# Kernel tuning notes

Measured on AMD Instinct MI355X. Metric: run time of the kernel, lower is better.

Reference implementation:

```python
import jax, jax.numpy as jnp
import numpy as np

D_MODEL = 1024
N_HEADS = 16
HEAD_DIM = D_MODEL // N_HEADS  # 64


def _rotate_half(x):
    x1, x2 = jnp.split(x, 2, axis=-1)
    return jnp.concatenate((-x2, x1), axis=-1)


def setup_inputs() -> dict:
    key = jax.random.key(0)
    ks = jax.random.split(key, 9)
    B, S = 2, 2048
    sc = 1.0 / np.sqrt(D_MODEL)
    return {
        "x": jax.random.normal(ks[0], (B, S, D_MODEL), dtype=jnp.float32),
        "Wq": jax.random.normal(ks[1], (D_MODEL, D_MODEL), dtype=jnp.float32) * sc,
        "bq": jax.random.normal(ks[2], (D_MODEL,), dtype=jnp.float32) * 0.02,
        "Wk": jax.random.normal(ks[3], (D_MODEL, D_MODEL), dtype=jnp.float32) * sc,
        "bk": jax.random.normal(ks[4], (D_MODEL,), dtype=jnp.float32) * 0.02,
        "Wv": jax.random.normal(ks[5], (D_MODEL, D_MODEL), dtype=jnp.float32) * sc,
        "bv": jax.random.normal(ks[6], (D_MODEL,), dtype=jnp.float32) * 0.02,
        "Wo": jax.random.normal(ks[7], (D_MODEL, D_MODEL), dtype=jnp.float32) * sc,
        "bo": jax.random.normal(ks[8], (D_MODEL,), dtype=jnp.float32) * 0.02,
    }


def reference(x, Wq, bq, Wk, bk, Wv, bv, Wo, bo):
    B, S, _ = x.shape
    H, D = N_HEADS, HEAD_DIM
    # QKV projections -> [B, H, S, D]
    q = (x @ Wq + bq).reshape(B, S, H, D).transpose(0, 2, 1, 3)
    k = (x @ Wk + bk).reshape(B, S, H, D).transpose(0, 2, 1, 3)
    v = (x @ Wv + bv).reshape(B, S, H, D).transpose(0, 2, 1, 3)
    # Rotary embedding on head_dim
    inv_freq = 1.0 / (10000.0 ** (jnp.arange(0, D, 2, dtype=jnp.float32) / D))
    t = jnp.arange(S, dtype=jnp.float32)
    freqs = jnp.outer(t, inv_freq)                      # [S, D/2]
    emb = jnp.concatenate((freqs, freqs), axis=-1)      # [S, D]
    # Faithful to torch: cos/sin end up rank-5 [1,1,1,S,D], promoting q/k to [1,B,H,S,D]
    cos = jnp.cos(emb)[None, None, None]
    sin = jnp.sin(emb)[None, None, None]
    qe = q * cos + _rotate_half(q) * sin                # [1,B,H,S,D]
    ke = k * cos + _rotate_half(k) * sin                # [1,B,H,S,D]
    scores = jnp.matmul(qe, jnp.swapaxes(ke, -1, -2)) / np.sqrt(D).astype(np.float32)  # [1,B,H,S,S]
    attn = jax.nn.softmax(scores, axis=-1)
    out = jnp.matmul(attn, v)                           # [1,B,H,S,D] (v broadcast)
    # Faithful replication of torch transpose(1,2).contiguous().view(B,S,d_model)
    out = out.transpose(0, 2, 1, 3, 4).reshape(B, S, H * D)
    return out @ Wo + bo
```

## Files before the change

### kernel.cpp

```cpp
#include <hip/hip_runtime.h>
#include <hip/hip_bf16.h>
#include <stdint.h>

typedef __bf16 bf16;
typedef __bf16 bf16x8 __attribute__((ext_vector_type(8)));
typedef __bf16 bf16x4 __attribute__((ext_vector_type(4)));
typedef float  f32x4  __attribute__((ext_vector_type(4)));
typedef int    i32x4  __attribute__((ext_vector_type(4)));

#define MFMA16(a, b, c) __builtin_amdgcn_mfma_f32_16x16x32_bf16((a), (b), (c), 0, 0, 0)

#define GLOAD16(gp, lp) __builtin_amdgcn_global_load_lds(                     \
    (__attribute__((address_space(1))) void*)(gp),                            \
    (__attribute__((address_space(3))) void*)(lp), 16, 0, 0)


__global__ __launch_bounds__(256) void k_prep(
    const float* __restrict__ x,
    const float* __restrict__ Wq, const float* __restrict__ Wk,
    const float* __restrict__ Wv, const float* __restrict__ Wo,
    bf16* __restrict__ xb, bf16* __restrict__ wqkvt, bf16* __restrict__ wot,
    float* __restrict__ ct, float* __restrict__ st) {
    __shared__ float t[32][33];
    const int bid = blockIdx.x, tid = threadIdx.x;
    if (bid < 4096) {
        const int i = bid * 256 + tid;
        float4 v = ((const float4*)x)[i];
        bf16x4 o;
        o[0] = (bf16)v.x; o[1] = (bf16)v.y; o[2] = (bf16)v.z; o[3] = (bf16)v.w;
        ((bf16x4*)xb)[i] = o;
    } else if (bid < 4352) {
        const int i = (bid - 4096) * 256 + tid;
        const int s = i >> 5, j = i & 31;
        const float inv = expf(-(float)j * (9.210340371976184f / 32.0f));
        const float a = (float)s * inv;
        ct[i] = cosf(a);
        st[i] = sinf(a);
    } else {
        const int wb = bid - 4352;
        const int z = wb >> 10, tb = wb & 1023;
        const float* src = (z == 0) ? Wq : (z == 1) ? Wk : (z == 2) ? Wv : Wo;
        bf16* dst = (z < 3) ? wqkvt + (size_t)z * 1024 * 1024 : wot;
        const int bx = (tb & 31) * 32, by = (tb >> 5) * 32;
        const int tx = tid & 31, ty = tid >> 5;
#pragma unroll
        for (int i = 0; i < 32; i += 8)
            t[ty + i][tx] = src[(size_t)(by + ty + i) * 1024 + bx + tx];
        __syncthreads();
#pragma unroll
        for (int i = 0; i < 32; i += 8)
            dst[(size_t)(bx + ty + i) * 1024 + by + tx] = (bf16)t[tx][ty + i];
    }
}

__device__ __forceinline__ void gemm_loop(const bf16* __restrict__ A,
                                          const bf16* __restrict__ Bt,
                                          int m0, int n0,
                                          bf16* As, bf16* Bs,
                                          f32x4 (&acc)[4][4]) {
    const int tid  = threadIdx.x;
    const int w    = tid >> 6, lane = tid & 63;
    const int wr   = (w >> 1) * 64, wc = (w & 1) * 64;
    const int l15  = lane & 15, l4 = lane >> 4;
    const int srow = w * 16 + (lane >> 2);
    const int skol = 8 * ((lane & 3) ^ ((lane >> 3) & 3));
    const int rdb  = l15 * 32 + 8 * (l4 ^ ((l15 >> 1) & 3));
    const bf16* Ap = A  + (size_t)(m0 + srow) * 1024 + skol;
    const bf16* Bp = Bt + (size_t)(n0 + srow) * 1024 + skol;

#define GSTAGE(B, kt) do {                                                   \
        GLOAD16(Ap + (kt),         As + (B) * 4096 + w * 512);               \
        GLOAD16(Ap + 65536 + (kt), As + (B) * 4096 + 2048 + w * 512);        \
        GLOAD16(Bp + (kt),         Bs + (B) * 4096 + w * 512);               \
        GLOAD16(Bp + 65536 + (kt), Bs + (B) * 4096 + 2048 + w * 512);        \
    } while (0)

#define GCOMP(B) do {                                                        \
        bf16x8 af[4], bfv[4];                                                \
        _Pragma("unroll")                                                    \
        for (int m = 0; m < 4; ++m)                                          \
            af[m] = *(const bf16x8*)(As + (B) * 4096 + (wr + 16 * m) * 32 + rdb); \
        _Pragma("unroll")                                                    \
        for (int n = 0; n < 4; ++n)                                          \
            bfv[n] = *(const bf16x8*)(Bs + (B) * 4096 + (wc + 16 * n) * 32 + rdb); \
        __builtin_amdgcn_s_setprio(1);                                       \
        _Pragma("unroll")                                                    \
        for (int m = 0; m < 4; ++m)                                          \
            _Pragma("unroll")                                                \
            for (int n = 0; n < 4; ++n)                                      \
                acc[m][n] = MFMA16(af[m], bfv[n], acc[m][n]);                \
        __builtin_amdgcn_s_setprio(0);                                       \
    } while (0)

    GSTAGE(0, 0);
    GSTAGE(1, 32);
    for (int i = 0; i < 30; i += 3) {
        asm volatile("s_waitcnt vmcnt(8)" ::: "memory");
        __builtin_amdgcn_s_barrier();
        GSTAGE(2, (i + 2) * 32);
        GCOMP(0);
        asm volatile("s_waitcnt vmcnt(8)" ::: "memory");
        __builtin_amdgcn_s_barrier();
        GSTAGE(0, (i + 3) * 32);
        GCOMP(1);
        asm volatile("s_waitcnt vmcnt(8)" ::: "memory");
        __builtin_amdgcn_s_barrier();
        GSTAGE(1, (i + 4) * 32);
        GCOMP(2);
    }
    asm volatile("s_waitcnt vmcnt(8)" ::: "memory");
    __builtin_amdgcn_s_barrier();
    GCOMP(0);
    asm volatile("s_waitcnt vmcnt(0)" ::: "memory");
    __builtin_amdgcn_s_barrier();
    GCOMP(1);
#undef GCOMP
#undef GSTAGE
}

__global__ __launch_bounds__(256) void k_gemm_qkv(
    const bf16* __restrict__ X, const bf16* __restrict__ Wt,
    const float* __restrict__ bq, const float* __restrict__ bk,
    const float* __restrict__ bv,
    const float* __restrict__ ct, const float* __restrict__ st,
    bf16* __restrict__ qbuf, bf16* __restrict__ kbuf, bf16* __restrict__ vtb) {
    __shared__ __align__(16) bf16 As[3 * 4096];
    __shared__ __align__(16) bf16 Bs[3 * 4096];
    f32x4 acc[4][4] = {};
    const int nwg = gridDim.x * gridDim.y;
    const int wg  = blockIdx.y * gridDim.x + blockIdx.x;
    const int sw  = (wg & 7) * (nwg >> 3) + (wg >> 3);
    const int m0 = (sw / gridDim.x) * 128, n0 = (sw % gridDim.x) * 128;
    gemm_loop(X, Wt, m0, n0, As, Bs, acc);

    const int tid = threadIdx.x;
    const int w = tid >> 6, lane = tid & 63;
    const int wr = (w >> 1) * 64, wc = (w & 1) * 64;
    const int l15 = lane & 15, l4 = lane >> 4;

    const int featbase = n0 + wc;
    const int kind = featbase >> 10;
    const int col0 = featbase & 1023;
    const int h = col0 >> 6;
    const float* bias = (kind == 0) ? bq : (kind == 1) ? bk : bv;
    const float oscale = (kind == 0) ? 0.18033688011112042f : 1.0f;

#pragma unroll
    for (int m = 0; m < 4; ++m) {
#pragma unroll
        for (int j = 0; j < 4; ++j) {
            const int tok = m0 + wr + 16 * m + 4 * l4 + j;
            const int b = tok >> 11, s = tok & 2047;
            float vals[4];
#pragma unroll
            for (int n = 0; n < 4; ++n)
                vals[n] = acc[m][n][j] + bias[col0 + 16 * n + l15];
            if (kind < 2) {
                bf16* dst = (kind == 0) ? qbuf : kbuf;
                const size_t base = ((size_t)((b * 16 + h) * 2048 + s)) * 64;
#pragma unroll
                for (int n = 0; n < 4; ++n) {
                    const int dd = 16 * n + l15;
                    const int jr = dd & 31;
                    const float c = ct[s * 32 + jr], sn = st[s * 32 + jr];
                    const float other = vals[n ^ 2];
                    const float rot = (dd < 32) ? -other : other;
                    dst[base + dd] = (bf16)((vals[n] * c + rot * sn) * oscale);
                }
            } else {
                const int sp = (s & ~63) | ((s & 0x1C) << 1) | ((s & 0x20) >> 3) | (s & 3);
#pragma unroll
                for (int n = 0; n < 4; ++n) {
                    const int dd = 16 * n + l15;
                    vtb[((size_t)((b * 16 + h) * 64 + dd)) * 2048 + sp] = (bf16)vals[n];
                }
            }
        }
    }
}

__global__ __launch_bounds__(512) void k_attn(const bf16* __restrict__ qbuf,
                                              const bf16* __restrict__ kbuf,
                                              const bf16* __restrict__ vtb,
                                              bf16* __restrict__ ob) {
    __shared__ __align__(16) bf16 smem[2 * 2 * 2 * 4096];

    const int tid = threadIdx.x, w = tid >> 6, lane = tid & 63;
    const int team = w >> 2, wt = w & 3;
    const int l15 = lane & 15, l4 = lane >> 4;

    const int sid = blockIdx.x;
    const int bh  = (sid & 7) * 4 + ((sid >> 3) >> 4);
    const int qb0 = ((sid >> 3) & 15) * 128;
    const int b = bh >> 4, h = bh & 15;

    const bf16* qp = qbuf + ((size_t)bh * 2048 + qb0 + wt * 32 + l15) * 64 + 8 * l4;
    i32x4 qr00 = *(const i32x4*)qp;
    i32x4 qr01 = *(const i32x4*)(qp + 32);
    i32x4 qr10 = *(const i32x4*)(qp + 16 * 64);
    i32x4 qr11 = *(const i32x4*)(qp + 16 * 64 + 32);
    asm volatile("" :: "v"(qr00), "v"(qr01), "v"(qr10), "v"(qr11));
    asm volatile("s_waitcnt vmcnt(0)" ::: "memory");
    bf16x8 aq[2][2];
    aq[0][0] = __builtin_bit_cast(bf16x8, qr00);
    aq[0][1] = __builtin_bit_cast(bf16x8, qr01);
    aq[1][0] = __builtin_bit_cast(bf16x8, qr10);
    aq[1][1] = __builtin_bit_cast(bf16x8, qr11);

    bf16x8 ones;
#pragma unroll
    for (int i = 0; i < 8; ++i) ones[i] = (bf16)1.0f;

    f32x4 ao[2][4] = {};
    f32x4 lacc[2] = {};
    const f32x4 zf = {0.f, 0.f, 0.f, 0.f};

    const int r8   = lane >> 3;
    const int skol = 8 * ((lane & 7) ^ r8);
    const int rdb  = l15 * 64 + 32 * ((l15 >> 2) & 1) + 8 * (l4 ^ (l15 & 3));
    const bf16* kp = kbuf + (size_t)bh * 131072 + (size_t)team * 65536
                   + (size_t)(wt * 8 + r8) * 64 + skol;
    const bf16* vp = vtb  + (size_t)bh * 131072 + (size_t)(wt * 8 + r8) * 2048
                   + team * 1024 + skol;
    bf16* sK = smem + team * 16384;
    bf16* sV = smem + team * 16384 + 8192;
    const bf16* pK0 = sK + rdb;
    const bf16* pK1 = sK + (rdb ^ 32);
    const bf16* pV0 = sV + rdb;
    const bf16* pV1 = sV + (rdb ^ 32);

#define STAGE(B, t) do {                                                  \
        GLOAD16(kp + (size_t)(t) * 4096,        sK + (B) * 4096 + wt * 512);        \
        GLOAD16(kp + (size_t)(t) * 4096 + 2048, sK + (B) * 4096 + 2048 + wt * 512); \
        GLOAD16(vp + (t) * 64,                  sV + (B) * 4096 + wt * 512);        \
        GLOAD16(vp + 65536 + (t) * 64,          sV + (B) * 4096 + 2048 + wt * 512); \
    } while (0)

#define TILE(t, B) do {                                                       \
        asm volatile("s_waitcnt vmcnt(0)" ::: "memory");                      \
        __builtin_amdgcn_s_barrier();                                         \
        if ((t) < 15) STAGE((B) ^ 1, (t) + 1);                                \
        bf16x8 kfr[2][4], vfr[2][4];                                          \
        _Pragma("unroll")                                                     \
        for (int n = 0; n < 4; ++n) {                                         \
            kfr[0][n] = *(const bf16x8*)(pK0 + (B) * 4096 + n * 1024);        \
            kfr[1][n] = *(const bf16x8*)(pK1 + (B) * 4096 + n * 1024);        \
            vfr[0][n] = *(const bf16x8*)(pV0 + (B) * 4096 + n * 1024);        \
            vfr[1][n] = *(const bf16x8*)(pV1 + (B) * 4096 + n * 1024);        \
        }                                                                     \
        f32x4 sc[2][4];                                                       \
        __builtin_amdgcn_s_setprio(1);                                        \
        _Pragma("unroll")                                                     \
        for (int n = 0; n < 4; ++n) {                                         \
            sc[0][n] = MFMA16(kfr[0][n], aq[0][0], zf);                       \
            sc[1][n] = MFMA16(kfr[0][n], aq[1][0], zf);                       \
        }                                                                     \
        _Pragma("unroll")                                                     \
        for (int n = 0; n < 4; ++n) {                                         \
            sc[0][n] = MFMA16(kfr[1][n], aq[0][1], sc[0][n]);                 \
            sc[1][n] = MFMA16(kfr[1][n], aq[1][1], sc[1][n]);                 \
        }                                                                     \
        __builtin_amdgcn_s_setprio(0);                                        \
                  \
        bf16x8 ap[2][2];                                                      \
        _Pragma("unroll")                                                     \
        for (int f = 0; f < 2; ++f) {                                         \
            float e0[4], e1[4], e2[4], e3[4];                                 \
            _Pragma("unroll")                                                 \
            for (int r = 0; r < 4; ++r) {                                     \
                asm("v_exp_f32 %0, %1" : "=v"(e0[r]) : "v"(sc[f][0][r]));     \
                asm("v_exp_f32 %0, %1" : "=v"(e1[r]) : "v"(sc[f][1][r]));     \
                asm("v_exp_f32 %0, %1" : "=v"(e2[r]) : "v"(sc[f][2][r]));     \
                asm("v_exp_f32 %0, %1" : "=v"(e3[r]) : "v"(sc[f][3][r]));     \
            }                                                                 \
            unsigned q0, q1, q2, q3, q4, q5, q6, q7;                          \
            asm("v_cvt_pk_bf16_f32 %0, %1, %2" : "=v"(q0) : "v"(e0[0]), "v"(e0[1])); \
            asm("v_cvt_pk_bf16_f32 %0, %1, %2" : "=v"(q1) : "v"(e0[2]), "v"(e0[3])); \
            asm("v_cvt_pk_bf16_f32 %0, %1, %2" : "=v"(q2) : "v"(e2[0]), "v"(e2[1])); \
            asm("v_cvt_pk_bf16_f32 %0, %1, %2" : "=v"(q3) : "v"(e2[2]), "v"(e2[3])); \
            asm("v_cvt_pk_bf16_f32 %0, %1, %2" : "=v"(q4) : "v"(e1[0]), "v"(e1[1])); \
            asm("v_cvt_pk_bf16_f32 %0, %1, %2" : "=v"(q5) : "v"(e1[2]), "v"(e1[3])); \
            asm("v_cvt_pk_bf16_f32 %0, %1, %2" : "=v"(q6) : "v"(e3[0]), "v"(e3[1])); \
            asm("v_cvt_pk_bf16_f32 %0, %1, %2" : "=v"(q7) : "v"(e3[2]), "v"(e3[3])); \
            i32x4 w0 = {(int)q0, (int)q1, (int)q2, (int)q3};                  \
            i32x4 w1 = {(int)q4, (int)q5, (int)q6, (int)q7};                  \
            ap[f][0] = __builtin_bit_cast(bf16x8, w0);                        \
            ap[f][1] = __builtin_bit_cast(bf16x8, w1);                        \
        }                                                                     \
        __builtin_amdgcn_s_setprio(1);                                        \
        lacc[0] = MFMA16(ap[0][0], ones, lacc[0]);                            \
        lacc[0] = MFMA16(ap[0][1], ones, lacc[0]);                            \
        lacc[1] = MFMA16(ap[1][0], ones, lacc[1]);                            \
        lacc[1] = MFMA16(ap[1][1], ones, lacc[1]);                            \
        _Pragma("unroll")                                                     \
        for (int kk = 0; kk < 2; ++kk)                                        \
            _Pragma("unroll")                                                 \
            for (int n = 0; n < 4; ++n) {                                     \
                ao[0][n] = MFMA16(ap[0][kk], vfr[kk][n], ao[0][n]);           \
                ao[1][n] = MFMA16(ap[1][kk], vfr[kk][n], ao[1][n]);           \
            }                                                                 \
        __builtin_amdgcn_s_setprio(0);                                        \
    } while (0)

    STAGE(0, 0);
    for (int t = 0; t < 16; t += 2) {
        TILE(t, 0);
        TILE(t + 1, 1);
    }
#undef TILE
#undef STAGE

    float* mO = (float*)(smem + 16384);
    float* mL = (float*)smem;
    __syncthreads();
    if (team == 1) {
#pragma unroll
        for (int f = 0; f < 2; ++f) {
#pragma unroll
            for (int j = 0; j < 4; ++j) {
                const int row = wt * 32 + f * 16 + 4 * l4 + j;
#pragma unroll
                for (int n = 0; n < 4; ++n)
                    mO[row * 64 + 16 * n + l15] = ao[f][n][j];
                if (l15 == 0) mL[row] = lacc[f][j];
            }
        }
    }
    __syncthreads();
    if (team == 0) {
#pragma unroll
        for (int f = 0; f < 2; ++f) {
#pragma unroll
            for (int j = 0; j < 4; ++j) {
                const int row = wt * 32 + f * 16 + 4 * l4 + j;
                const float inv = 1.0f / (lacc[f][j] + mL[row]);
                const int s = qb0 + row;
                const size_t base = ((size_t)(h * 256 + b * 128 + (s >> 4))) * 1024
                                  + (s & 15) * 64;
#pragma unroll
                for (int n = 0; n < 4; ++n)
                    ob[base + 16 * n + l15] =
                        (bf16)((ao[f][n][j] + mO[row * 64 + 16 * n + l15]) * inv);
            }
        }
    }
}

__global__ __launch_bounds__(256) void k_gemm_out(const bf16* __restrict__ O,
                                                  const bf16* __restrict__ Wt,
                                                  const float* __restrict__ bo,
                                                  float* __restrict__ out) {
    __shared__ __align__(16) bf16 As[3 * 4096];
    __shared__ __align__(16) bf16 Bs[3 * 4096];
    f32x4 acc[4][4] = {};
    const int nwg = gridDim.x * gridDim.y;
    const int wg  = blockIdx.y * gridDim.x + blockIdx.x;
    const int sw  = (wg & 7) * (nwg >> 3) + (wg >> 3);
    const int m0 = (sw / gridDim.x) * 128, n0 = (sw % gridDim.x) * 128;
    gemm_loop(O, Wt, m0, n0, As, Bs, acc);

    const int tid = threadIdx.x;
    const int w = tid >> 6, lane = tid & 63;
    const int wr = (w >> 1) * 64, wc = (w & 1) * 64;
    const int l15 = lane & 15, l4 = lane >> 4;
#pragma unroll
    for (int m = 0; m < 4; ++m) {
#pragma unroll
        for (int j = 0; j < 4; ++j) {
            const int tok = m0 + wr + 16 * m + 4 * l4 + j;
#pragma unroll
            for (int n = 0; n < 4; ++n) {
                const int feat = n0 + wc + 16 * n + l15;
                out[(size_t)tok * 1024 + feat] = acc[m][n][j] + bo[feat];
            }
        }
    }
}

extern "C" void kernel_launch(void* const* d_in, const int* in_sizes, int n_in,
                              void* d_out, int out_size, void* d_ws, size_t ws_size,
                              hipStream_t stream) {
    (void)in_sizes; (void)n_in; (void)out_size; (void)ws_size;
    const float* x  = (const float*)d_in[0];
    const float* Wq = (const float*)d_in[1];
    const float* bq = (const float*)d_in[2];
    const float* Wk = (const float*)d_in[3];
    const float* bk = (const float*)d_in[4];
    const float* Wv = (const float*)d_in[5];
    const float* bv = (const float*)d_in[6];
    const float* Wo = (const float*)d_in[7];
    const float* bo = (const float*)d_in[8];
    float* out = (float*)d_out;

    char* p = (char*)d_ws;
    bf16* xb    = (bf16*)p;  p += (size_t)4096 * 1024 * 2;
    bf16* wqkvt = (bf16*)p;  p += (size_t)3072 * 1024 * 2;
    bf16* wot   = (bf16*)p;  p += (size_t)1024 * 1024 * 2;
    bf16* qbuf  = (bf16*)p;  p += (size_t)32 * 2048 * 64 * 2;
    bf16* kbuf  = (bf16*)p;  p += (size_t)32 * 2048 * 64 * 2;
    bf16* vtb   = (bf16*)p;  p += (size_t)32 * 64 * 2048 * 2;
    float* ct   = (float*)p; p += (size_t)2048 * 32 * 4;
    float* st   = (float*)p; p += (size_t)2048 * 32 * 4;
    bf16* obuf  = xb;

    k_prep<<<dim3(8448), dim3(256), 0, stream>>>(x, Wq, Wk, Wv, Wo,
                                                 xb, wqkvt, wot, ct, st);
    k_gemm_qkv<<<dim3(24, 32), dim3(256), 0, stream>>>(xb, wqkvt, bq, bk, bv,
                                                       ct, st, qbuf, kbuf, vtb);
    k_attn<<<dim3(512), dim3(512), 0, stream>>>(qbuf, kbuf, vtb, obuf);
    k_gemm_out<<<dim3(8, 32), dim3(256), 0, stream>>>(obuf, wot, bo, out);
}
```

Measured before the change: 118.8 us.

## Widen QKV GEMM tile to 128x256 with per-wave 128x64 subtiles

Replaces the shared gemm_loop in the QKV projection with a dedicated 128x256 tile loop. Each wave now computes all 128 rows for its own 64-column slice, so the grid is halved to 12x32 blocks. Every wave keeps 8x4 accumulators and reads all A fragments from shared memory. The aim is to raise arithmetic intensity and reuse of A per loaded tile. The cost is more registers and LDS per block, fewer blocks, and lower occupancy, which could hurt the load balance across the 256 CUs.

```diff
diff --git a/kernel.cpp b/kernel.cpp
--- a/kernel.cpp
+++ b/kernel.cpp
@@ -125,20 +125,75 @@
     const float* __restrict__ ct, const float* __restrict__ st,
     bf16* __restrict__ qbuf, bf16* __restrict__ kbuf, bf16* __restrict__ vtb) {
     __shared__ __align__(16) bf16 As[3 * 4096];
-    __shared__ __align__(16) bf16 Bs[3 * 4096];
-    f32x4 acc[4][4] = {};
+    __shared__ __align__(16) bf16 Bs[3 * 8192];
+    f32x4 acc[8][4] = {};
+
     const int nwg = gridDim.x * gridDim.y;
     const int wg  = blockIdx.y * gridDim.x + blockIdx.x;
     const int sw  = (wg & 7) * (nwg >> 3) + (wg >> 3);
-    const int m0 = (sw / gridDim.x) * 128, n0 = (sw % gridDim.x) * 128;
-    gemm_loop(X, Wt, m0, n0, As, Bs, acc);
-
-    const int tid = threadIdx.x;
-    const int w = tid >> 6, lane = tid & 63;
-    const int wr = (w >> 1) * 64, wc = (w & 1) * 64;
-    const int l15 = lane & 15, l4 = lane >> 4;
-
-    const int featbase = n0 + wc;
+    const int n0 = (sw % gridDim.x) * 256, m0 = (sw / gridDim.x) * 128;
+
+    const int tid  = threadIdx.x;
+    const int w    = tid >> 6, lane = tid & 63;
+    const int l15  = lane & 15, l4 = lane >> 4;
+    const int srow = w * 16 + (lane >> 2);
+    const int skol = 8 * ((lane & 3) ^ ((lane >> 3) & 3));
+    const int rdb  = l15 * 32 + 8 * (l4 ^ ((l15 >> 1) & 3));
+    const bf16* Ap = X  + (size_t)(m0 + srow) * 1024 + skol;
+    const bf16* Bp = Wt + (size_t)(n0 + srow) * 1024 + skol;
+
+#define WSTAGE(B, kt) do {                                                   \
+        GLOAD16(Ap + (kt),          As + (B) * 4096 + w * 512);              \
+        GLOAD16(Ap + 65536 + (kt),  As + (B) * 4096 + 2048 + w * 512);       \
+        GLOAD16(Bp + (kt),          Bs + (B) * 8192 + w * 512);              \
+        GLOAD16(Bp + 65536 + (kt),  Bs + (B) * 8192 + 2048 + w * 512);       \
+        GLOAD16(Bp + 131072 + (kt), Bs + (B) * 8192 + 4096 + w * 512);       \
+        GLOAD16(Bp + 196608 + (kt), Bs + (B) * 8192 + 6144 + w * 512);       \
+    } while (0)
+
+#define WCOMP(B) do {                                                        \
+        bf16x8 bfv[4], af[8];                                                \
+        _Pragma("unroll")                                                    \
+        for (int n = 0; n < 4; ++n)                                          \
+            bfv[n] = *(const bf16x8*)(Bs + (B) * 8192 + w * 2048 + n * 512 + rdb); \
+        _Pragma("unroll")                                                    \
+        for (int m = 0; m < 8; ++m)                                          \
+            af[m] = *(const bf16x8*)(As + (B) * 4096 + m * 512 + rdb);       \
+        __builtin_amdgcn_s_setprio(1);                                       \
+        _Pragma("unroll")                                                    \
+        for (int m = 0; m < 8; ++m)                                          \
+            _Pragma("unroll")                                                \
+            for (int n = 0; n < 4; ++n)                                      \
+                acc[m][n] = MFMA16(af[m], bfv[n], acc[m][n]);                \
+        __builtin_amdgcn_s_setprio(0);                                       \
+    } while (0)
+
+    WSTAGE(0, 0);
+    WSTAGE(1, 32);
+    for (int i = 0; i < 30; i += 3) {
+        asm volatile("s_waitcnt vmcnt(6)" ::: "memory");
+        __builtin_amdgcn_s_barrier();
+        WSTAGE(2, (i + 2) * 32);
+        WCOMP(0);
+        asm volatile("s_waitcnt vmcnt(6)" ::: "memory");
+        __builtin_amdgcn_s_barrier();
+        WSTAGE(0, (i + 3) * 32);
+        WCOMP(1);
+        asm volatile("s_waitcnt vmcnt(6)" ::: "memory");
+        __builtin_amdgcn_s_barrier();
+        WSTAGE(1, (i + 4) * 32);
+        WCOMP(2);
+    }
+    asm volatile("s_waitcnt vmcnt(6)" ::: "memory");
+    __builtin_amdgcn_s_barrier();
+    WCOMP(0);
+    asm volatile("s_waitcnt vmcnt(0)" ::: "memory");
+    __builtin_amdgcn_s_barrier();
+    WCOMP(1);
+#undef WCOMP
+#undef WSTAGE
+
+    const int featbase = n0 + w * 64;
     const int kind = featbase >> 10;
     const int col0 = featbase & 1023;
     const int h = col0 >> 6;
@@ -146,10 +201,10 @@
     const float oscale = (kind == 0) ? 0.18033688011112042f : 1.0f;
 
 #pragma unroll
-    for (int m = 0; m < 4; ++m) {
+    for (int m = 0; m < 8; ++m) {
 #pragma unroll
         for (int j = 0; j < 4; ++j) {
-            const int tok = m0 + wr + 16 * m + 4 * l4 + j;
+            const int tok = m0 + 16 * m + 4 * l4 + j;
             const int b = tok >> 11, s = tok & 2047;
             float vals[4];
 #pragma unroll
@@ -405,7 +460,7 @@
 
     k_prep<<<dim3(8448), dim3(256), 0, stream>>>(x, Wq, Wk, Wv, Wo,
                                                  xb, wqkvt, wot, ct, st);
-    k_gemm_qkv<<<dim3(24, 32), dim3(256), 0, stream>>>(xb, wqkvt, bq, bk, bv,
+    k_gemm_qkv<<<dim3(12, 32), dim3(256), 0, stream>>>(xb, wqkvt, bq, bk, bv,
                                                        ct, st, qbuf, kbuf, vtb);
     k_attn<<<dim3(512), dim3(512), 0, stream>>>(qbuf, kbuf, vtb, obuf);
     k_gemm_out<<<dim3(8, 32), dim3(256), 0, stream>>>(obuf, wot, bo, out);
```

After: 151.4 us. 1.27x slower.
